# Performance work log

Measured on AMD Instinct MI355X. Metric: run time of the kernel, lower is better.

The kernel has to match this reference:

```python
import jax, jax.numpy as jnp
import numpy as np

B, T, IN, H, L, OUT, PRED, FN = 512, 96, 64, 512, 2, 1, 24, 32


def setup_inputs() -> dict:
    key = jax.random.key(0)
    ks = jax.random.split(key, 12)
    sc = 0.02
    n = lambda i, shape: jax.random.normal(ks[i], shape, jnp.float32) * sc
    return {
        "x": jax.random.normal(ks[0], (B, T, IN), jnp.float32),
        "station_id": jax.random.randint(ks[1], (B,), 0, 26, jnp.int32),
        "W_hidden": n(2, (H, IN)), "b_hidden": jnp.zeros((H,), jnp.float32),
        "embed": n(3, (26, H)),
        "W_ih": n(4, (L, 4 * H, H)), "W_hh": n(5, (L, 4 * H, H)),
        "b_ih": jnp.zeros((L, 4 * H), jnp.float32), "b_hh": jnp.zeros((L, 4 * H), jnp.float32),
        "conv_W": n(6, (FN, T - 1)), "conv_b": jnp.zeros((FN,), jnp.float32),
        "W1": n(7, (FN, H)), "b1": jnp.zeros((FN,), jnp.float32),
        "W2": n(8, (H, H + FN)), "b2": jnp.zeros((H,), jnp.float32),
        "W_out": n(9, (T * OUT, H)), "b_out": jnp.zeros((T * OUT,), jnp.float32),
    }


def _lstm(xc, W_ih, W_hh, b_ih, b_hh):
    # xc: [B, T, H]; multi-layer LSTM, PyTorch gate order i,f,g,o
    n_layers = W_ih.shape[0]
    h0 = jnp.zeros((n_layers, xc.shape[0], W_hh.shape[-1]), xc.dtype)

    def step(carry, xt):
        h, c = carry  # [L, B, H]
        inp = xt
        hs, cs = [], []
        for l in range(n_layers):
            g = inp @ W_ih[l].T + h[l] @ W_hh[l].T + b_ih[l] + b_hh[l]
            i, f, gg, o = jnp.split(g, 4, axis=-1)
            cn = jax.nn.sigmoid(f) * c[l] + jax.nn.sigmoid(i) * jnp.tanh(gg)
            hn = jax.nn.sigmoid(o) * jnp.tanh(cn)
            hs.append(hn); cs.append(cn)
            inp = hn
        return (jnp.stack(hs), jnp.stack(cs)), inp  # emit last-layer h

    _, outs = jax.lax.scan(step, (h0, h0), jnp.swapaxes(xc, 0, 1))
    return jnp.swapaxes(outs, 0, 1)  # [B, T, H] last-layer hidden states


def reference(x, station_id, W_hidden, b_hidden, embed, W_ih, W_hh, b_ih, b_hh,
              conv_W, conv_b, W1, b1, W2, b2, W_out, b_out):
    b, t, _ = x.shape
    hdim = W_hidden.shape[0]
    fn = conv_W.shape[0]
    xc = jax.nn.relu(x @ W_hidden.T + b_hidden)
    xc = xc + embed[station_id][:, None, :]
    hs_seq = _lstm(xc, W_ih, W_hh, b_ih, b_hh)          # [B, T, H]
    Hmat = jax.nn.relu(hs_seq[:, :-1, :])                # [B, T-1, H]
    htt = hs_seq[:, -1, :]                               # [B, H]
    # Conv2d(1, FN, (T-1, 1)) over [B,1,T-1,H] == contraction over time
    conv = jax.nn.relu(jnp.einsum('bth,ft->bfh', Hmat, conv_W) + conv_b[None, :, None])
    # original does .view(-1, feat_size, filter_num): raw reshape, not transpose
    feat = conv.reshape(b, hdim, fn)                     # [B, H, FN]
    w = (htt @ W1.T + b1)[:, None, :]                    # [B, 1, FN]
    alpha = jax.nn.sigmoid(jnp.sum(feat * w, axis=2))    # [B, H]
    v = jnp.sum(alpha[:, :, None] * feat, axis=1)        # [B, FN]
    new_ht = jnp.concatenate([htt, v], axis=1) @ W2.T + b2
    ypred = (new_ht @ W_out.T + b_out)[:, -PRED * OUT:]
    return ypred
```

## Files before the change

### kernel.cpp

```cpp
#include <hip/hip_runtime.h>
#include <math.h>

namespace {

constexpr int B = 512, T = 96, IN = 64, H = 512, G4 = 2048;
constexpr int FN = 32, KC = 544, NPRED = 24, TM1 = T - 1;
constexpr int BH = B * H;

typedef __attribute__((ext_vector_type(8))) short s8v;
typedef __attribute__((ext_vector_type(16))) float f16v;

__device__ __forceinline__ float sigf(float x) { return 1.0f / (1.0f + __expf(-x)); }
__device__ __forceinline__ float tanhfast(float x) {
  x = fminf(fmaxf(x, -15.f), 15.f);
  float e = __expf(2.0f * x);
  return (e - 1.0f) / (e + 1.0f);
}
__device__ __forceinline__ unsigned short bf16_rne(float f) {
  unsigned u = __float_as_uint(f);
  u += 0x7fffu + ((u >> 16) & 1u);
  return (unsigned short)(u >> 16);
}
__device__ __forceinline__ void split8(const float4& x, const float4& y, s8v& hi, s8v& lo) {
  float vs[8] = {x.x, x.y, x.z, x.w, y.x, y.y, y.z, y.w};
#pragma unroll
  for (int j = 0; j < 8; ++j) {
    unsigned ub = __float_as_uint(vs[j]);
    hi[j] = (short)(ub >> 16);
    lo[j] = (short)bf16_rne(vs[j] - __uint_as_float(ub & 0xffff0000u));
  }
}

__global__ __launch_bounds__(256) void k_xc(
    const float* __restrict__ x, const int* __restrict__ sid,
    const float* __restrict__ Wh, const float* __restrict__ bh,
    const float* __restrict__ emb, float* __restrict__ planes) {
  constexpr int RB = 8;
  int row0 = blockIdx.x * RB;
  int tid = threadIdx.x;
  __shared__ float sW[IN][257];
  __shared__ int ssid[RB];
  if (tid < RB) ssid[tid] = sid[(row0 + tid) / T];
  for (int hc = 0; hc < 2; ++hc) {
    __syncthreads();
    for (int i = tid; i < 256 * IN; i += 256) {
      int h = i >> 6, k = i & 63;
      sW[k][h] = Wh[(size_t)(hc * 256 + h) * IN + k];
    }
    __syncthreads();
    int h = hc * 256 + tid;
    float b0 = bh[h];
    float acc[RB];
#pragma unroll
    for (int r = 0; r < RB; ++r) acc[r] = b0;
#pragma unroll 4
    for (int kc = 0; kc < IN / 4; ++kc) {
      float4 xv[RB];
#pragma unroll
      for (int r = 0; r < RB; ++r)
        xv[r] = *(const float4*)(x + (size_t)(row0 + r) * IN + kc * 4);
      float w0 = sW[kc * 4 + 0][tid];
      float w1 = sW[kc * 4 + 1][tid];
      float w2 = sW[kc * 4 + 2][tid];
      float w3 = sW[kc * 4 + 3][tid];
#pragma unroll
      for (int r = 0; r < RB; ++r) {
        acc[r] = fmaf(xv[r].x, w0, acc[r]);
        acc[r] = fmaf(xv[r].y, w1, acc[r]);
        acc[r] = fmaf(xv[r].z, w2, acc[r]);
        acc[r] = fmaf(xv[r].w, w3, acc[r]);
      }
    }
#pragma unroll
    for (int r = 0; r < RB; ++r) {
      int row = row0 + r;
      int bb = row / T, t = row % T;
      float v = fmaxf(acc[r], 0.f) + emb[(size_t)ssid[r] * H + h];
      planes[((size_t)t * B + bb) * H + h] = v;
    }
  }
}

__global__ __launch_bounds__(256) void k_wswz(
    const float* __restrict__ Wih, const float* __restrict__ Whh,
    short* __restrict__ WFhi, short* __restrict__ WFlo) {
  int g = blockIdx.x * 256 + threadIdx.x;
  int lane = g & 63;
  int fi = g >> 6;
  int nt = fi & 3, kt = (fi >> 2) & 63, ng = (fi >> 8) & 15, layer = fi >> 12;
  int row = nt * H + ng * 32 + (lane & 31);
  int kk = kt * 16 + (lane >> 5) * 8;
  const float* src = (kk < H) ? (Wih + ((size_t)layer * G4 + row) * H + kk)
                              : (Whh + ((size_t)layer * G4 + row) * H + (kk - H));
  float4 f0 = *(const float4*)src, f1 = *(const float4*)(src + 4);
  s8v hi, lo;
  split8(f0, f1, hi, lo);
  size_t o = (size_t)fi * 512 + lane * 8;
  *(s8v*)(WFhi + o) = hi;
  *(s8v*)(WFlo + o) = lo;
}

__global__ __launch_bounds__(256, 2) void k_step(
    int tt, float* __restrict__ planes, const short* __restrict__ WFhi,
    const short* __restrict__ WFlo, short* __restrict__ hFhi,
    short* __restrict__ hFlo, const float* __restrict__ bih,
    const float* __restrict__ bhh, float* __restrict__ c0,
    float* __restrict__ c1) {
  int gid = blockIdx.x;
  int xcd = gid & 7;
  int u = gid >> 3;
  int v = u & 31, aa = u >> 5;
  int layer = v >> 4;
  if (layer ? (tt == 0) : (tt == T)) return;
  int ng = xcd * 2 + ((v >> 3) & 1);
  int bg = (v & 7) | (aa << 3);
  int b0 = bg * 32;
  int step = layer ? (tt - 1) : tt;
  int tid = threadIdx.x, lane = tid & 63, wk = tid >> 6;
  int l31 = lane & 31, lh = lane >> 5;

  __shared__ float comb[4][4][32][32];

  const float* bi = bih + (size_t)layer * G4;
  const float* bh2 = bhh + (size_t)layer * G4;
  float* cbuf = layer ? c1 : c0;

  int rpar = (step - 1) & 1;
  const float* xbase = nullptr;
  const short *abhi = nullptr, *ablo = nullptr;
  if (layer == 0 && wk < 2) {
    xbase = planes + (size_t)step * BH + (size_t)(b0 + l31) * H + wk * 256 + lh * 8;
  } else {
    int src = (layer == 0) ? 0 : ((wk < 2) ? 0 : 1);
    int par = (layer == 0) ? rpar : ((wk < 2) ? (step & 1) : rpar);
    int kk0 = wk * 16 - ((layer == 0 || wk >= 2) ? 32 : 0);
    size_t o = ((((size_t)src * 2 + par) * 32 + kk0) * H + (b0 + l31)) * 16 + lh * 8;
    abhi = hFhi + o;
    ablo = hFlo + o;
  }

  float bias[4];
#pragma unroll
  for (int nt = 0; nt < 4; ++nt) {
    int r = nt * H + ng * 32 + l31;
    bias[nt] = bi[r] + bh2[r];
  }

  const size_t wstep = 4 * 512;
  const size_t wbase0 = ((size_t)(layer * 16 + ng) * 64 + wk * 16) * wstep + (size_t)lane * 8;
  const size_t astep = (size_t)H * 16;

  f16v acc[4];
#pragma unroll
  for (int nt = 0; nt < 4; ++nt)
#pragma unroll
    for (int e = 0; e < 16; ++e) acc[nt][e] = 0.f;

  s8v a0h, a0l, b0h0, b0h1, b0h2, b0h3, b0l0, b0l1, b0l2, b0l3;
  s8v a1h, a1l, b1h0, b1h1, b1h2, b1h3, b1l0, b1l1, b1l2, b1l3;
  s8v a2h, a2l, b2h0, b2h1, b2h2, b2h3, b2l0, b2l1, b2l2, b2l3;

#define LOADW_(kq, bh0, bh1, bh2, bh3, bl0, bl1, bl2, bl3)          \
  {                                                                 \
    size_t wo = wbase0 + (size_t)(kq) * wstep;                      \
    bh0 = *(const s8v*)(WFhi + wo);                                 \
    bh1 = *(const s8v*)(WFhi + wo + 512);                           \
    bh2 = *(const s8v*)(WFhi + wo + 1024);                          \
    bh3 = *(const s8v*)(WFhi + wo + 1536);                          \
    bl0 = *(const s8v*)(WFlo + wo);                                 \
    bl1 = *(const s8v*)(WFlo + wo + 512);                           \
    bl2 = *(const s8v*)(WFlo + wo + 1024);                          \
    bl3 = *(const s8v*)(WFlo + wo + 1536);                          \
  }
#define LOADA_(kq, ah, al)                                          \
  {                                                                 \
    if (xbase) {                                                    \
      const float* ap = xbase + (kq) * 16;                          \
      float4 f0 = *(const float4*)ap, f1 = *(const float4*)(ap + 4);\
      split8(f0, f1, ah, al);                                       \
    } else {                                                        \
      ah = *(const s8v*)(abhi + (size_t)(kq) * astep);              \
      al = *(const s8v*)(ablo + (size_t)(kq) * astep);              \
    }                                                               \
  }
#define MFMA3_(ah, al, bh0, bh1, bh2, bh3, bl0, bl1, bl2, bl3)                         \
  {                                                                                    \
    acc[0] = __builtin_amdgcn_mfma_f32_32x32x16_bf16(ah, bh0, acc[0], 0, 0, 0);        \
    acc[1] = __builtin_amdgcn_mfma_f32_32x32x16_bf16(ah, bh1, acc[1], 0, 0, 0);        \
    acc[2] = __builtin_amdgcn_mfma_f32_32x32x16_bf16(ah, bh2, acc[2], 0, 0, 0);        \
    acc[3] = __builtin_amdgcn_mfma_f32_32x32x16_bf16(ah, bh3, acc[3], 0, 0, 0);        \
    acc[0] = __builtin_amdgcn_mfma_f32_32x32x16_bf16(ah, bl0, acc[0], 0, 0, 0);        \
    acc[1] = __builtin_amdgcn_mfma_f32_32x32x16_bf16(ah, bl1, acc[1], 0, 0, 0);        \
    acc[2] = __builtin_amdgcn_mfma_f32_32x32x16_bf16(ah, bl2, acc[2], 0, 0, 0);        \
    acc[3] = __builtin_amdgcn_mfma_f32_32x32x16_bf16(ah, bl3, acc[3], 0, 0, 0);        \
    acc[0] = __builtin_amdgcn_mfma_f32_32x32x16_bf16(al, bh0, acc[0], 0, 0, 0);        \
    acc[1] = __builtin_amdgcn_mfma_f32_32x32x16_bf16(al, bh1, acc[1], 0, 0, 0);        \
    acc[2] = __builtin_amdgcn_mfma_f32_32x32x16_bf16(al, bh2, acc[2], 0, 0, 0);        \
    acc[3] = __builtin_amdgcn_mfma_f32_32x32x16_bf16(al, bh3, acc[3], 0, 0, 0);        \
  }

  LOADA_(0, a0h, a0l);
  LOADW_(0, b0h0, b0h1, b0h2, b0h3, b0l0, b0l1, b0l2, b0l3);
  LOADA_(1, a1h, a1l);
  LOADW_(1, b1h0, b1h1, b1h2, b1h3, b1l0, b1l1, b1l2, b1l3);
  LOADA_(2, a2h, a2l);
  LOADW_(2, b2h0, b2h1, b2h2, b2h3, b2l0, b2l1, b2l2, b2l3);
#pragma unroll 1
  for (int kp = 0; kp < 5; ++kp) {
    int kq = kp * 3;
    MFMA3_(a0h, a0l, b0h0, b0h1, b0h2, b0h3, b0l0, b0l1, b0l2, b0l3);
    LOADA_(kq + 3, a0h, a0l);
    LOADW_(kq + 3, b0h0, b0h1, b0h2, b0h3, b0l0, b0l1, b0l2, b0l3);
    MFMA3_(a1h, a1l, b1h0, b1h1, b1h2, b1h3, b1l0, b1l1, b1l2, b1l3);
    if (kp < 4) {
      LOADA_(kq + 4, a1h, a1l);
      LOADW_(kq + 4, b1h0, b1h1, b1h2, b1h3, b1l0, b1l1, b1l2, b1l3);
    }
    MFMA3_(a2h, a2l, b2h0, b2h1, b2h2, b2h3, b2l0, b2l1, b2l2, b2l3);
    if (kp < 4) {
      LOADA_(kq + 5, a2h, a2l);
      LOADW_(kq + 5, b2h0, b2h1, b2h2, b2h3, b2l0, b2l1, b2l2, b2l3);
    }
  }
  MFMA3_(a0h, a0l, b0h0, b0h1, b0h2, b0h3, b0l0, b0l1, b0l2, b0l3);
#undef LOADW_
#undef LOADA_
#undef MFMA3_

#pragma unroll
  for (int nt = 0; nt < 4; ++nt)
#pragma unroll
    for (int r = 0; r < 16; ++r) {
      int row = (r & 3) + 8 * (r >> 2) + 4 * lh;
      comb[nt][wk][row][l31] = acc[nt][r];
    }
  __syncthreads();
#pragma unroll
  for (int rr = 0; rr < 4; ++rr) {
    int r = wk * 4 + rr;
    int row = (r & 3) + 8 * (r >> 2) + 4 * lh;
    float g[4];
#pragma unroll
    for (int nt = 0; nt < 4; ++nt) {
      float p0 = comb[nt][0][row][l31];
      float p1 = comb[nt][1][row][l31];
      float p2 = comb[nt][2][row][l31];
      float p3 = comb[nt][3][row][l31];
      g[nt] = (p0 + p1) + (p2 + p3) + bias[nt];
    }
    size_t coff = (size_t)(b0 + row) * H + ng * 32 + l31;
    float cp = cbuf[coff];
    float cn = sigf(g[1]) * cp + sigf(g[0]) * tanhfast(g[2]);
    float hn = sigf(g[3]) * tanhfast(cn);
    cbuf[coff] = cn;
    int brow = b0 + row;
    int hcol = ng * 32 + l31;
    size_t o = ((((size_t)layer * 2 + (step & 1)) * 32 + (hcol >> 4)) * H + brow) * 16 + (hcol & 15);
    unsigned ub = __float_as_uint(hn);
    hFhi[o] = (short)(ub >> 16);
    hFlo[o] = (short)bf16_rne(hn - __uint_as_float(ub & 0xffff0000u));
    if (layer) planes[(size_t)step * BH + (size_t)brow * H + hcol] = hn;
  }
}

__global__ __launch_bounds__(256) void k_conv(
    const float* __restrict__ hs, const float* __restrict__ cW,
    const float* __restrict__ cb, float* __restrict__ feat) {
  int b = blockIdx.x >> 2;
  int h0 = (blockIdx.x & 3) * 128;
  int tid = threadIdx.x;
  __shared__ float sW[TM1][FN];
  for (int i = tid; i < TM1 * FN; i += 256) sW[i >> 5][i & 31] = cW[(i & 31) * TM1 + (i >> 5)];
  __syncthreads();
  int hl = tid & 127, fg = (tid >> 7) * 16;
  float acc[16];
#pragma unroll
  for (int j = 0; j < 16; ++j) acc[j] = cb[fg + j];
  const float* hp = hs + (size_t)b * H + h0 + hl;
  for (int t = 0; t < TM1; ++t) {
    float v = fmaxf(hp[(size_t)t * BH], 0.f);
#pragma unroll
    for (int j = 0; j < 16; ++j) acc[j] = fmaf(v, sW[t][fg + j], acc[j]);
  }
#pragma unroll
  for (int j = 0; j < 16; ++j)
    feat[(size_t)b * (FN * H) + (size_t)(fg + j) * H + h0 + hl] = fmaxf(acc[j], 0.f);
}

__global__ __launch_bounds__(256) void k_attn(
    const float* __restrict__ hs, const float* __restrict__ feat,
    const float* __restrict__ W1, const float* __restrict__ b1,
    const float* __restrict__ W2, const float* __restrict__ b2,
    const float* __restrict__ Wout, const float* __restrict__ bout,
    float* __restrict__ out) {
  int b = blockIdx.x, tid = threadIdx.x;
  __shared__ float sh[H], sa[H], snew[H], sw[FN], sv[FN], red[256];
  const float* htt = hs + (size_t)(T - 1) * BH + (size_t)b * H;
  for (int i = tid; i < H; i += 256) sh[i] = htt[i];
  __syncthreads();
  {
    int f = tid >> 3, sl = tid & 7;
    const float* w1 = W1 + (size_t)f * H;
    float p = 0.f;
    for (int k = sl * 64; k < sl * 64 + 64; ++k) p = fmaf(sh[k], w1[k], p);
    p += __shfl_xor(p, 1); p += __shfl_xor(p, 2); p += __shfl_xor(p, 4);
    if (sl == 0) sw[f] = p + b1[f];
  }
  __syncthreads();
  const float* fb = feat + (size_t)b * (FN * H);
  for (int i = tid; i < H; i += 256) {
    const float* fr = fb + (size_t)i * FN;
    float p = 0.f;
#pragma unroll
    for (int j = 0; j < FN; j += 4) {
      float4 fv = *(const float4*)(fr + j);
      p = fmaf(fv.x, sw[j], p);
      p = fmaf(fv.y, sw[j + 1], p);
      p = fmaf(fv.z, sw[j + 2], p);
      p = fmaf(fv.w, sw[j + 3], p);
    }
    sa[i] = sigf(p);
  }
  __syncthreads();
  {
    int j = tid & 31, isl = tid >> 5;
    float p = 0.f;
    for (int i = isl * 64; i < isl * 64 + 64; ++i) p = fmaf(sa[i], fb[(size_t)i * FN + j], p);
    red[tid] = p;
  }
  __syncthreads();
  if (tid < 128) red[tid] += red[tid + 128];
  __syncthreads();
  if (tid < 64) red[tid] += red[tid + 64];
  __syncthreads();
  if (tid < 32) sv[tid] = red[tid] + red[tid + 32];
  __syncthreads();
  for (int h = tid; h < H; h += 256) {
    const float* w2 = W2 + (size_t)h * KC;
    float p = b2[h];
#pragma unroll 4
    for (int k = 0; k < H; k += 4) {
      float4 wv = *(const float4*)(w2 + k);
      float4 shv = *(const float4*)(sh + k);
      p = fmaf(shv.x, wv.x, p);
      p = fmaf(shv.y, wv.y, p);
      p = fmaf(shv.z, wv.z, p);
      p = fmaf(shv.w, wv.w, p);
    }
#pragma unroll
    for (int j = 0; j < FN; j += 4) {
      float4 wv = *(const float4*)(w2 + H + j);
      p = fmaf(sv[j], wv.x, p);
      p = fmaf(sv[j + 1], wv.y, p);
      p = fmaf(sv[j + 2], wv.z, p);
      p = fmaf(sv[j + 3], wv.w, p);
    }
    snew[h] = p;
  }
  __syncthreads();
  if (tid < NPRED * 8) {
    int p = tid >> 3, sl = tid & 7;
    const float* wo = Wout + (size_t)(T - NPRED + p) * H;
    float sacc = 0.f;
    for (int k = sl * 64; k < sl * 64 + 64; ++k) sacc = fmaf(snew[k], wo[k], sacc);
    sacc += __shfl_xor(sacc, 1); sacc += __shfl_xor(sacc, 2); sacc += __shfl_xor(sacc, 4);
    if (sl == 0) out[(size_t)b * NPRED + p] = sacc + bout[T - NPRED + p];
  }
}

}

extern "C" void kernel_launch(void* const* d_in, const int* in_sizes, int n_in,
                              void* d_out, int out_size, void* d_ws, size_t ws_size,
                              hipStream_t stream) {
  const float* x    = (const float*)d_in[0];
  const int*   sid  = (const int*)d_in[1];
  const float* Wh   = (const float*)d_in[2];
  const float* bh   = (const float*)d_in[3];
  const float* emb  = (const float*)d_in[4];
  const float* Wih  = (const float*)d_in[5];
  const float* Whh  = (const float*)d_in[6];
  const float* bih  = (const float*)d_in[7];
  const float* bhh  = (const float*)d_in[8];
  const float* cW   = (const float*)d_in[9];
  const float* cb   = (const float*)d_in[10];
  const float* W1   = (const float*)d_in[11];
  const float* b1   = (const float*)d_in[12];
  const float* W2   = (const float*)d_in[13];
  const float* b2   = (const float*)d_in[14];
  const float* Wout = (const float*)d_in[15];
  const float* bout = (const float*)d_in[16];
  float* out = (float*)d_out;

  constexpr size_t HFE = (size_t)2 * 2 * 32 * H * 16;
  float* planes = (float*)d_ws;
  short* WFhi = (short*)(planes + (size_t)T * BH);
  short* WFlo = WFhi + (size_t)8192 * 512;
  short* hFhi = WFlo + (size_t)8192 * 512;
  short* hFlo = hFhi + HFE;
  float* cst = (float*)(hFlo + HFE);
  float* c0 = cst;
  float* c1 = cst + BH;
  float* feat = c1 + BH;
  size_t need = (size_t)T * BH * 4 + (size_t)8192 * 512 * 2 * 2 + HFE * 2 * 2 +
                2 * (size_t)BH * 4 + (size_t)B * FN * H * 4;
  if (ws_size < need) return;

  hipMemsetAsync(hFhi, 0, HFE * 2 * 2 + 2 * (size_t)BH * 4, stream);
  k_xc<<<(B * T) / 8, 256, 0, stream>>>(x, sid, Wh, bh, emb, planes);
  k_wswz<<<2048, 256, 0, stream>>>(Wih, Whh, WFhi, WFlo);

  for (int tt = 0; tt <= T; ++tt)
    k_step<<<512, 256, 0, stream>>>(tt, planes, WFhi, WFlo, hFhi, hFlo, bih, bhh, c0, c1);

  k_conv<<<B * 4, 256, 0, stream>>>(planes, cW, cb, feat);
  k_attn<<<B, 256, 0, stream>>>(planes, feat, W1, b1, W2, b2, Wout, bout, out);
}
```

Before: 2.417 ms.

## Double batch rows per LSTM step block to reuse weight fragments; restructure xc projection

Each k_step block now handles 64 batch rows (two 32-row MFMA tiles) instead of 32, so every loaded weight fragment feeds twice as many MFMAs. The grid is halved to 256 blocks with launch bounds of 1 block per SM, and the block-to-(layer, gate group, batch) mapping is remapped. This cuts global weight traffic per step but doubles accumulator registers and lowers the number of blocks in flight. The input projection kernel is also rewritten to keep each thread's weight row in registers and stage 64 x rows in shared memory, which removes the transposed weight staging in shared memory.

```diff
diff --git a/kernel.cpp b/kernel.cpp
--- a/kernel.cpp
+++ b/kernel.cpp
@@ -35,49 +35,41 @@
     const float* __restrict__ x, const int* __restrict__ sid,
     const float* __restrict__ Wh, const float* __restrict__ bh,
     const float* __restrict__ emb, float* __restrict__ planes) {
-  constexpr int RB = 8;
-  int row0 = blockIdx.x * RB;
+  constexpr int RWS = 64;
+  int gid = blockIdx.x;
+  int half = gid & 1;
+  int row0 = (gid >> 1) * RWS;
   int tid = threadIdx.x;
-  __shared__ float sW[IN][257];
-  __shared__ int ssid[RB];
-  if (tid < RB) ssid[tid] = sid[(row0 + tid) / T];
-  for (int hc = 0; hc < 2; ++hc) {
-    __syncthreads();
-    for (int i = tid; i < 256 * IN; i += 256) {
-      int h = i >> 6, k = i & 63;
-      sW[k][h] = Wh[(size_t)(hc * 256 + h) * IN + k];
-    }
-    __syncthreads();
-    int h = hc * 256 + tid;
-    float b0 = bh[h];
-    float acc[RB];
-#pragma unroll
-    for (int r = 0; r < RB; ++r) acc[r] = b0;
-#pragma unroll 4
-    for (int kc = 0; kc < IN / 4; ++kc) {
-      float4 xv[RB];
-#pragma unroll
-      for (int r = 0; r < RB; ++r)
-        xv[r] = *(const float4*)(x + (size_t)(row0 + r) * IN + kc * 4);
-      float w0 = sW[kc * 4 + 0][tid];
-      float w1 = sW[kc * 4 + 1][tid];
-      float w2 = sW[kc * 4 + 2][tid];
-      float w3 = sW[kc * 4 + 3][tid];
-#pragma unroll
-      for (int r = 0; r < RB; ++r) {
-        acc[r] = fmaf(xv[r].x, w0, acc[r]);
-        acc[r] = fmaf(xv[r].y, w1, acc[r]);
-        acc[r] = fmaf(xv[r].z, w2, acc[r]);
-        acc[r] = fmaf(xv[r].w, w3, acc[r]);
-      }
-    }
-#pragma unroll
-    for (int r = 0; r < RB; ++r) {
-      int row = row0 + r;
-      int bb = row / T, t = row % T;
-      float v = fmaxf(acc[r], 0.f) + emb[(size_t)ssid[r] * H + h];
-      planes[((size_t)t * B + bb) * H + h] = v;
-    }
+  int h = half * 256 + tid;
+  __shared__ float sx[RWS][IN];
+  {
+    const float4* xsrc = (const float4*)(x + (size_t)row0 * IN);
+    float4* sdst = (float4*)(&sx[0][0]);
+    for (int i = tid; i < RWS * IN / 4; i += 256) sdst[i] = xsrc[i];
+  }
+  float4 w[16];
+  const float* wr = Wh + (size_t)h * IN;
+#pragma unroll
+  for (int j = 0; j < 16; ++j) w[j] = *(const float4*)(wr + j * 4);
+  float b0 = bh[h];
+  const float* ep = emb + h;
+  __syncthreads();
+#pragma unroll 2
+  for (int r = 0; r < RWS; ++r) {
+    float a0 = b0, a1 = 0.f, a2 = 0.f, a3 = 0.f;
+#pragma unroll
+    for (int j = 0; j < 16; ++j) {
+      float4 xv = *(const float4*)(&sx[r][j * 4]);
+      a0 = fmaf(xv.x, w[j].x, a0);
+      a1 = fmaf(xv.y, w[j].y, a1);
+      a2 = fmaf(xv.z, w[j].z, a2);
+      a3 = fmaf(xv.w, w[j].w, a3);
+    }
+    float acc = (a0 + a1) + (a2 + a3);
+    int row = row0 + r;
+    int bb = row / T, t = row % T;
+    float v = fmaxf(acc, 0.f) + ep[(size_t)sid[bb] * H];
+    planes[((size_t)t * B + bb) * H + h] = v;
   }
 }
 
@@ -100,7 +92,7 @@
   *(s8v*)(WFlo + o) = lo;
 }
 
-__global__ __launch_bounds__(256, 2) void k_step(
+__global__ __launch_bounds__(256, 1) void k_step(
     int tt, float* __restrict__ planes, const short* __restrict__ WFhi,
     const short* __restrict__ WFlo, short* __restrict__ hFhi,
     short* __restrict__ hFlo, const float* __restrict__ bih,
@@ -109,12 +101,11 @@
   int gid = blockIdx.x;
   int xcd = gid & 7;
   int u = gid >> 3;
-  int v = u & 31, aa = u >> 5;
-  int layer = v >> 4;
+  int combo = xcd * 4 + (u & 3);
+  int layer = combo >> 4;
   if (layer ? (tt == 0) : (tt == T)) return;
-  int ng = xcd * 2 + ((v >> 3) & 1);
-  int bg = (v & 7) | (aa << 3);
-  int b0 = bg * 32;
+  int ng = combo & 15;
+  int b0 = (u >> 2) * 64;
   int step = layer ? (tt - 1) : tt;
   int tid = threadIdx.x, lane = tid & 63, wk = tid >> 6;
   int l31 = lane & 31, lh = lane >> 5;
@@ -150,15 +141,17 @@
   const size_t wbase0 = ((size_t)(layer * 16 + ng) * 64 + wk * 16) * wstep + (size_t)lane * 8;
   const size_t astep = (size_t)H * 16;
 
-  f16v acc[4];
-#pragma unroll
-  for (int nt = 0; nt < 4; ++nt)
-#pragma unroll
-    for (int e = 0; e < 16; ++e) acc[nt][e] = 0.f;
-
-  s8v a0h, a0l, b0h0, b0h1, b0h2, b0h3, b0l0, b0l1, b0l2, b0l3;
-  s8v a1h, a1l, b1h0, b1h1, b1h2, b1h3, b1l0, b1l1, b1l2, b1l3;
-  s8v a2h, a2l, b2h0, b2h1, b2h2, b2h3, b2l0, b2l1, b2l2, b2l3;
+  f16v acc[2][4];
+#pragma unroll
+  for (int rt = 0; rt < 2; ++rt)
+#pragma unroll
+    for (int nt = 0; nt < 4; ++nt)
+#pragma unroll
+      for (int e = 0; e < 16; ++e) acc[rt][nt][e] = 0.f;
+
+  s8v a0h0, a0l0, a0h1, a0l1, b0h0, b0h1, b0h2, b0h3, b0l0, b0l1, b0l2, b0l3;
+  s8v a1h0, a1l0, a1h1, a1l1, b1h0, b1h1, b1h2, b1h3, b1l0, b1l1, b1l2, b1l3;
+  s8v a2h0, a2l0, a2h1, a2l1, b2h0, b2h1, b2h2, b2h3, b2l0, b2l1, b2l2, b2l3;
 
 #define LOADW_(kq, bh0, bh1, bh2, bh3, bl0, bl1, bl2, bl3)          \
   {                                                                 \
@@ -172,94 +165,112 @@
     bl2 = *(const s8v*)(WFlo + wo + 1024);                          \
     bl3 = *(const s8v*)(WFlo + wo + 1536);                          \
   }
-#define LOADA_(kq, ah, al)                                          \
+#define LOADA_(kq, ah0, al0, ah1, al1)                              \
   {                                                                 \
     if (xbase) {                                                    \
       const float* ap = xbase + (kq) * 16;                          \
       float4 f0 = *(const float4*)ap, f1 = *(const float4*)(ap + 4);\
-      split8(f0, f1, ah, al);                                       \
+      split8(f0, f1, ah0, al0);                                     \
+      const float* aq = ap + 32 * H;                                \
+      float4 g0 = *(const float4*)aq, g1 = *(const float4*)(aq + 4);\
+      split8(g0, g1, ah1, al1);                                     \
     } else {                                                        \
-      ah = *(const s8v*)(abhi + (size_t)(kq) * astep);              \
-      al = *(const s8v*)(ablo + (size_t)(kq) * astep);              \
+      const short* ph = abhi + (size_t)(kq) * astep;                \
+      const short* pl = ablo + (size_t)(kq) * astep;                \
+      ah0 = *(const s8v*)(ph);                                      \
+      al0 = *(const s8v*)(pl);                                      \
+      ah1 = *(const s8v*)(ph + 512);                                \
+      al1 = *(const s8v*)(pl + 512);                                \
     }                                                               \
   }
-#define MFMA3_(ah, al, bh0, bh1, bh2, bh3, bl0, bl1, bl2, bl3)                         \
-  {                                                                                    \
-    acc[0] = __builtin_amdgcn_mfma_f32_32x32x16_bf16(ah, bh0, acc[0], 0, 0, 0);        \
-    acc[1] = __builtin_amdgcn_mfma_f32_32x32x16_bf16(ah, bh1, acc[1], 0, 0, 0);        \
-    acc[2] = __builtin_amdgcn_mfma_f32_32x32x16_bf16(ah, bh2, acc[2], 0, 0, 0);        \
-    acc[3] = __builtin_amdgcn_mfma_f32_32x32x16_bf16(ah, bh3, acc[3], 0, 0, 0);        \
-    acc[0] = __builtin_amdgcn_mfma_f32_32x32x16_bf16(ah, bl0, acc[0], 0, 0, 0);        \
-    acc[1] = __builtin_amdgcn_mfma_f32_32x32x16_bf16(ah, bl1, acc[1], 0, 0, 0);        \
-    acc[2] = __builtin_amdgcn_mfma_f32_32x32x16_bf16(ah, bl2, acc[2], 0, 0, 0);        \
-    acc[3] = __builtin_amdgcn_mfma_f32_32x32x16_bf16(ah, bl3, acc[3], 0, 0, 0);        \
-    acc[0] = __builtin_amdgcn_mfma_f32_32x32x16_bf16(al, bh0, acc[0], 0, 0, 0);        \
-    acc[1] = __builtin_amdgcn_mfma_f32_32x32x16_bf16(al, bh1, acc[1], 0, 0, 0);        \
-    acc[2] = __builtin_amdgcn_mfma_f32_32x32x16_bf16(al, bh2, acc[2], 0, 0, 0);        \
-    acc[3] = __builtin_amdgcn_mfma_f32_32x32x16_bf16(al, bh3, acc[3], 0, 0, 0);        \
-  }
-
-  LOADA_(0, a0h, a0l);
+#define MFMA3R_(rt, ah, al, bh0, bh1, bh2, bh3, bl0, bl1, bl2, bl3)                        \
+  {                                                                                        \
+    acc[rt][0] = __builtin_amdgcn_mfma_f32_32x32x16_bf16(ah, bh0, acc[rt][0], 0, 0, 0);    \
+    acc[rt][1] = __builtin_amdgcn_mfma_f32_32x32x16_bf16(ah, bh1, acc[rt][1], 0, 0, 0);    \
+    acc[rt][2] = __builtin_amdgcn_mfma_f32_32x32x16_bf16(ah, bh2, acc[rt][2], 0, 0, 0);    \
+    acc[rt][3] = __builtin_amdgcn_mfma_f32_32x32x16_bf16(ah, bh3, acc[rt][3], 0, 0, 0);    \
+    acc[rt][0] = __builtin_amdgcn_mfma_f32_32x32x16_bf16(ah, bl0, acc[rt][0], 0, 0, 0);    \
+    acc[rt][1] = __builtin_amdgcn_mfma_f32_32x32x16_bf16(ah, bl1, acc[rt][1], 0, 0, 0);    \
+    acc[rt][2] = __builtin_amdgcn_mfma_f32_32x32x16_bf16(ah, bl2, acc[rt][2], 0, 0, 0);    \
+    acc[rt][3] = __builtin_amdgcn_mfma_f32_32x32x16_bf16(ah, bl3, acc[rt][3], 0, 0, 0);    \
+    acc[rt][0] = __builtin_amdgcn_mfma_f32_32x32x16_bf16(al, bh0, acc[rt][0], 0, 0, 0);    \
+    acc[rt][1] = __builtin_amdgcn_mfma_f32_32x32x16_bf16(al, bh1, acc[rt][1], 0, 0, 0);    \
+    acc[rt][2] = __builtin_amdgcn_mfma_f32_32x32x16_bf16(al, bh2, acc[rt][2], 0, 0, 0);    \
+    acc[rt][3] = __builtin_amdgcn_mfma_f32_32x32x16_bf16(al, bh3, acc[rt][3], 0, 0, 0);    \
+  }
+#define MFMA6_(ah0, al0, ah1, al1, bh0, bh1, bh2, bh3, bl0, bl1, bl2, bl3)  \
+  {                                                                         \
+    MFMA3R_(0, ah0, al0, bh0, bh1, bh2, bh3, bl0, bl1, bl2, bl3);           \
+    MFMA3R_(1, ah1, al1, bh0, bh1, bh2, bh3, bl0, bl1, bl2, bl3);           \
+  }
+
+  LOADA_(0, a0h0, a0l0, a0h1, a0l1);
   LOADW_(0, b0h0, b0h1, b0h2, b0h3, b0l0, b0l1, b0l2, b0l3);
-  LOADA_(1, a1h, a1l);
+  LOADA_(1, a1h0, a1l0, a1h1, a1l1);
   LOADW_(1, b1h0, b1h1, b1h2, b1h3, b1l0, b1l1, b1l2, b1l3);
-  LOADA_(2, a2h, a2l);
+  LOADA_(2, a2h0, a2l0, a2h1, a2l1);
   LOADW_(2, b2h0, b2h1, b2h2, b2h3, b2l0, b2l1, b2l2, b2l3);
 #pragma unroll 1
   for (int kp = 0; kp < 5; ++kp) {
     int kq = kp * 3;
-    MFMA3_(a0h, a0l, b0h0, b0h1, b0h2, b0h3, b0l0, b0l1, b0l2, b0l3);
-    LOADA_(kq + 3, a0h, a0l);
+    MFMA6_(a0h0, a0l0, a0h1, a0l1, b0h0, b0h1, b0h2, b0h3, b0l0, b0l1, b0l2, b0l3);
+    LOADA_(kq + 3, a0h0, a0l0, a0h1, a0l1);
     LOADW_(kq + 3, b0h0, b0h1, b0h2, b0h3, b0l0, b0l1, b0l2, b0l3);
-    MFMA3_(a1h, a1l, b1h0, b1h1, b1h2, b1h3, b1l0, b1l1, b1l2, b1l3);
+    MFMA6_(a1h0, a1l0, a1h1, a1l1, b1h0, b1h1, b1h2, b1h3, b1l0, b1l1, b1l2, b1l3);
     if (kp < 4) {
-      LOADA_(kq + 4, a1h, a1l);
+      LOADA_(kq + 4, a1h0, a1l0, a1h1, a1l1);
       LOADW_(kq + 4, b1h0, b1h1, b1h2, b1h3, b1l0, b1l1, b1l2, b1l3);
     }
-    MFMA3_(a2h, a2l, b2h0, b2h1, b2h2, b2h3, b2l0, b2l1, b2l2, b2l3);
+    MFMA6_(a2h0, a2l0, a2h1, a2l1, b2h0, b2h1, b2h2, b2h3, b2l0, b2l1, b2l2, b2l3);
     if (kp < 4) {
-      LOADA_(kq + 5, a2h, a2l);
+      LOADA_(kq + 5, a2h0, a2l0, a2h1, a2l1);
       LOADW_(kq + 5, b2h0, b2h1, b2h2, b2h3, b2l0, b2l1, b2l2, b2l3);
     }
   }
-  MFMA3_(a0h, a0l, b0h0, b0h1, b0h2, b0h3, b0l0, b0l1, b0l2, b0l3);
+  MFMA6_(a0h0, a0l0, a0h1, a0l1, b0h0, b0h1, b0h2, b0h3, b0l0, b0l1, b0l2, b0l3);
 #undef LOADW_
 #undef LOADA_
-#undef MFMA3_
-
-#pragma unroll
-  for (int nt = 0; nt < 4; ++nt)
-#pragma unroll
-    for (int r = 0; r < 16; ++r) {
+#undef MFMA3R_
+#undef MFMA6_
+
+#pragma unroll
+  for (int rt = 0; rt < 2; ++rt) {
+    if (rt) __syncthreads();
+#pragma unroll
+    for (int nt = 0; nt < 4; ++nt)
+#pragma unroll
+      for (int r = 0; r < 16; ++r) {
+        int row = (r & 3) + 8 * (r >> 2) + 4 * lh;
+        comb[nt][wk][row][l31] = acc[rt][nt][r];
+      }
+    __syncthreads();
+    int b0p = b0 + rt * 32;
+#pragma unroll
+    for (int rr = 0; rr < 4; ++rr) {
+      int r = wk * 4 + rr;
       int row = (r & 3) + 8 * (r >> 2) + 4 * lh;
-      comb[nt][wk][row][l31] = acc[nt][r];
-    }
-  __syncthreads();
-#pragma unroll
-  for (int rr = 0; rr < 4; ++rr) {
-    int r = wk * 4 + rr;
-    int row = (r & 3) + 8 * (r >> 2) + 4 * lh;
-    float g[4];
-#pragma unroll
-    for (int nt = 0; nt < 4; ++nt) {
-      float p0 = comb[nt][0][row][l31];
-      float p1 = comb[nt][1][row][l31];
-      float p2 = comb[nt][2][row][l31];
-      float p3 = comb[nt][3][row][l31];
-      g[nt] = (p0 + p1) + (p2 + p3) + bias[nt];
-    }
-    size_t coff = (size_t)(b0 + row) * H + ng * 32 + l31;
-    float cp = cbuf[coff];
-    float cn = sigf(g[1]) * cp + sigf(g[0]) * tanhfast(g[2]);
-    float hn = sigf(g[3]) * tanhfast(cn);
-    cbuf[coff] = cn;
-    int brow = b0 + row;
-    int hcol = ng * 32 + l31;
-    size_t o = ((((size_t)layer * 2 + (step & 1)) * 32 + (hcol >> 4)) * H + brow) * 16 + (hcol & 15);
-    unsigned ub = __float_as_uint(hn);
-    hFhi[o] = (short)(ub >> 16);
-    hFlo[o] = (short)bf16_rne(hn - __uint_as_float(ub & 0xffff0000u));
-    if (layer) planes[(size_t)step * BH + (size_t)brow * H + hcol] = hn;
+      float g[4];
+#pragma unroll
+      for (int nt = 0; nt < 4; ++nt) {
+        float p0 = comb[nt][0][row][l31];
+        float p1 = comb[nt][1][row][l31];
+        float p2 = comb[nt][2][row][l31];
+        float p3 = comb[nt][3][row][l31];
+        g[nt] = (p0 + p1) + (p2 + p3) + bias[nt];
+      }
+      size_t coff = (size_t)(b0p + row) * H + ng * 32 + l31;
+      float cp = cbuf[coff];
+      float cn = sigf(g[1]) * cp + sigf(g[0]) * tanhfast(g[2]);
+      float hn = sigf(g[3]) * tanhfast(cn);
+      cbuf[coff] = cn;
+      int brow = b0p + row;
+      int hcol = ng * 32 + l31;
+      size_t o = ((((size_t)layer * 2 + (step & 1)) * 32 + (hcol >> 4)) * H + brow) * 16 + (hcol & 15);
+      unsigned ub = __float_as_uint(hn);
+      hFhi[o] = (short)(ub >> 16);
+      hFlo[o] = (short)bf16_rne(hn - __uint_as_float(ub & 0xffff0000u));
+      if (layer) planes[(size_t)step * BH + (size_t)brow * H + hcol] = hn;
+    }
   }
 }
 
@@ -407,11 +418,11 @@
   if (ws_size < need) return;
 
   hipMemsetAsync(hFhi, 0, HFE * 2 * 2 + 2 * (size_t)BH * 4, stream);
-  k_xc<<<(B * T) / 8, 256, 0, stream>>>(x, sid, Wh, bh, emb, planes);
+  k_xc<<<(B * T / 64) * 2, 256, 0, stream>>>(x, sid, Wh, bh, emb, planes);
   k_wswz<<<2048, 256, 0, stream>>>(Wih, Whh, WFhi, WFlo);
 
   for (int tt = 0; tt <= T; ++tt)
-    k_step<<<512, 256, 0, stream>>>(tt, planes, WFhi, WFlo, hFhi, hFlo, bih, bhh, c0, c1);
+    k_step<<<256, 256, 0, stream>>>(tt, planes, WFhi, WFlo, hFhi, hFlo, bih, bhh, c0, c1);
 
   k_conv<<<B * 4, 256, 0, stream>>>(planes, cW, cb, feat);
   k_attn<<<B, 256, 0, stream>>>(planes, feat, W1, b1, W2, b2, Wout, bout, out);
```

After: 2.324 ms. 3.8% less time.
